# Optimization experiments

Measured on AMD Instinct MI355X. Metric: run time of the kernel, lower is better.

The kernel has to match this reference:

```python
import jax, jax.numpy as jnp
import numpy as np

B, T, H, E = 8, 2048, 512, 512

def setup_inputs() -> dict:
    key = jax.random.key(0)
    k1, k2, k3, k4 = jax.random.split(key, 4)
    tokens = jax.random.normal(k1, (B, T, H), dtype=jnp.float32)
    # Linear(hidden,embed,bias=False): stored as (in,out) so Q = tokens @ Wq
    Wq = jax.random.normal(k2, (H, E), dtype=jnp.float32) / np.sqrt(H)
    Wk = jax.random.normal(k3, (H, E), dtype=jnp.float32) / np.sqrt(H)
    Wv = jax.random.normal(k4, (H, H), dtype=jnp.float32) / np.sqrt(H)
    return {"tokens": tokens, "Wq": Wq, "Wk": Wk, "Wv": Wv}

def reference(tokens, Wq, Wk, Wv):
    Q = jnp.einsum('bth,he->bte', tokens, Wq)   # [B,T,E]
    K = jnp.einsum('bsh,he->bse', tokens, Wk)   # [B,T,E]
    V = jnp.einsum('bsh,hd->bsd', tokens, Wv)   # [B,T,H]
    scoremats = jnp.einsum('bte,bse->bts', Q, K)  # [B,T,T]
    # NOTE: softmax over axis=1 (query axis t), matching F.softmax(dim=1)
    attnmats = jax.nn.softmax(scoremats, axis=1)
    ctx_vecs = jnp.einsum('bts,bsh->bth', attnmats, V)  # [B,T,H]
    return ctx_vecs
```

## Files before the change

kernel.cpp:

```cpp
#include <hip/hip_runtime.h>

typedef _Float16 f16;
typedef _Float16 f16x8 __attribute__((ext_vector_type(8)));
typedef _Float16 f16x4 __attribute__((ext_vector_type(4)));
typedef float   f32x4 __attribute__((ext_vector_type(4)));

#define LOG2E 1.44269504088896340736f

__device__ __forceinline__ f32x4 mfma_f16(f16x8 a, f16x8 b, f32x4 c){
  return __builtin_amdgcn_mfma_f32_16x16x32_f16(a, b, c, 0, 0, 0);
}
__device__ __forceinline__ float fexp2(float x){ return __builtin_amdgcn_exp2f(x); }

__device__ __forceinline__ void gld16(void* lds, const void* g){
  __builtin_amdgcn_global_load_lds(
      (const __attribute__((address_space(1))) unsigned int*)g,
      (__attribute__((address_space(3))) unsigned int*)lds,
      16, 0, 0);
}


__global__ __launch_bounds__(256) void k_prep_g(const float* __restrict__ Wq,
                                                const float* __restrict__ Wk,
                                                f16* __restrict__ B16){
  __shared__ float ak[32][36];
  __shared__ float aq[32][36];
  const int n0 = blockIdx.y * 32, e0 = blockIdx.x * 32;
  const int u = threadIdx.x;
  const int ty = u >> 4, tx = u & 15;
  float acc[2][2] = {};
  for (int x0 = 0; x0 < 512; x0 += 32){
    __syncthreads();
    {
      int r = u >> 3, c4 = (u & 7) * 4;
      *(float4*)&ak[r][c4] = *(const float4*)&Wk[(n0 + r) * 512 + x0 + c4];
      *(float4*)&aq[r][c4] = *(const float4*)&Wq[(e0 + r) * 512 + x0 + c4];
    }
    __syncthreads();
#pragma unroll 8
    for (int x = 0; x < 32; ++x){
      float k0 = ak[ty * 2 + 0][x], k1 = ak[ty * 2 + 1][x];
      float q0 = aq[tx * 2 + 0][x], q1 = aq[tx * 2 + 1][x];
      acc[0][0] += k0 * q0; acc[0][1] += k0 * q1;
      acc[1][0] += k1 * q0; acc[1][1] += k1 * q1;
    }
  }
#pragma unroll
  for (int i = 0; i < 2; ++i)
#pragma unroll
    for (int j = 0; j < 2; ++j)
      B16[(size_t)(n0 + ty * 2 + i) * 512 + e0 + tx * 2 + j] = (f16)acc[i][j];
}

__global__ __launch_bounds__(256) void k_prep_wv(const float* __restrict__ Wv,
                                                 f16* __restrict__ B16){
  __shared__ float t[64][72];
  const int e0 = blockIdx.x * 64, h0 = blockIdx.y * 64;
  const int u = threadIdx.x;
#pragma unroll
  for (int k = 0; k < 4; ++k){
    int idx = u + k * 256; int r = idx >> 4, c4 = (idx & 15) * 4;
    *(float4*)&t[r][c4] = *(const float4*)&Wv[(e0 + r) * 512 + h0 + c4];
  }
  __syncthreads();
#pragma unroll
  for (int k = 0; k < 4; ++k){
    int idx = u + k * 256; int j = idx >> 4, i4 = (idx & 15) * 4;
#pragma unroll
    for (int c = 0; c < 4; ++c)
      B16[(size_t)(512 + h0 + j) * 512 + e0 + i4 + c] = (f16)t[i4 + c][j];
  }
}

__global__ __launch_bounds__(256) void k_cast(const float* __restrict__ tok,
                                              f16* __restrict__ T16){
  int i = blockIdx.x * 256 + threadIdx.x;
  const float4* p = (const float4*)tok + (size_t)i * 2;
  float4 a = p[0], b = p[1];
  f16x8 h;
  h[0] = (f16)a.x; h[1] = (f16)a.y; h[2] = (f16)a.z; h[3] = (f16)a.w;
  h[4] = (f16)b.x; h[5] = (f16)b.y; h[6] = (f16)b.z; h[7] = (f16)b.w;
  *((f16x8*)T16 + i) = h;
}

__global__ __launch_bounds__(256, 4) void k_gemm(const f16* __restrict__ T16,
                                                 const f16* __restrict__ B16,
                                                 f16* __restrict__ QG,
                                                 f16* __restrict__ VT){
  __shared__ __align__(16) f16 Abuf[2][128 * 32];
  __shared__ __align__(16) f16 Bbuf[2][128 * 32];
  const int tb = blockIdx.x, nb = blockIdx.y;
  const int u = threadIdx.x;
  const int w = u >> 6, l = u & 63, lr = l & 15, lq = l >> 4;
  const int sxor = (l & 3) ^ ((l >> 3) & 3), hi4 = l >> 2;
  const int wm = (w & 1) * 64, wn = (w >> 1) * 64;
  f32x4 acc[4][4] = {};
  auto stage = [&](int c, int buf){
    const f16* sa = T16 + (size_t)tb * 128 * 512 + c * 32;
    const f16* sb = B16 + (size_t)nb * 128 * 512 + c * 32;
#pragma unroll
    for (int k = 0; k < 2; ++k){
      int i = w * 2 + k;
      int row = i * 16 + hi4;
      gld16((char*)&Abuf[buf][0] + i * 1024, sa + (size_t)row * 512 + sxor * 8);
      gld16((char*)&Bbuf[buf][0] + i * 1024, sb + (size_t)row * 512 + sxor * 8);
    }
  };
  stage(0, 0);
  for (int c = 0; c < 16; ++c){
    __syncthreads();
    if (c < 15) stage(c + 1, (c + 1) & 1);
    const f16* A = &Abuf[c & 1][0];
    const f16* B = &Bbuf[c & 1][0];
    f16x8 af[4], bf[4];
#pragma unroll
    for (int mt = 0; mt < 4; ++mt){
      int row = wm + mt * 16 + lr;
      af[mt] = *(const f16x8*)((const char*)A + row * 64 + (((lq ^ ((row >> 1) & 3))) << 4));
    }
#pragma unroll
    for (int nt = 0; nt < 4; ++nt){
      int row = wn + nt * 16 + lr;
      bf[nt] = *(const f16x8*)((const char*)B + row * 64 + (((lq ^ ((row >> 1) & 3))) << 4));
    }
#pragma unroll
    for (int mt = 0; mt < 4; ++mt)
#pragma unroll
      for (int nt = 0; nt < 4; ++nt)
        acc[mt][nt] = mfma_f16(af[mt], bf[nt], acc[mt][nt]);
  }
  if (nb < 4){
#pragma unroll
    for (int mt = 0; mt < 4; ++mt)
#pragma unroll
      for (int nt = 0; nt < 4; ++nt){
        int n = nb * 128 + wn + nt * 16 + lr;
        int r0 = tb * 128 + wm + mt * 16 + lq * 4;
#pragma unroll
        for (int j = 0; j < 4; ++j)
          QG[(size_t)(r0 + j) * 512 + n] = (f16)acc[mt][nt][j];
      }
  } else {
#pragma unroll
    for (int mt = 0; mt < 4; ++mt)
#pragma unroll
      for (int nt = 0; nt < 4; ++nt){
        int h = (nb - 4) * 128 + wn + nt * 16 + lr;
        int r0 = tb * 128 + wm + mt * 16 + lq * 4;
        int bq = r0 >> 11, s = r0 & 2047;
        f16x4 hv;
#pragma unroll
        for (int j = 0; j < 4; ++j) hv[j] = (f16)acc[mt][nt][j];
        *(f16x4*)&VT[(size_t)(bq * 512 + h) * 2048 + s] = hv;
      }
  }
}

__global__ __launch_bounds__(256, 4) void k_pass1p(const f16* __restrict__ T16,
                                                   const f16* __restrict__ QG,
                                                   f16* __restrict__ Pp,
                                                   float* __restrict__ Mp,
                                                   float* __restrict__ Dp){
  const int gid = blockIdx.x;
  const int b = gid & 7;
  const int sb = (gid >> 3) & 15;
  const int tb = gid >> 7;
  const int u = threadIdx.x;
  const int w = u >> 6, l = u & 63, lr = l & 15, lq = l >> 4;
  const int sxor = (l & 3) ^ ((l >> 3) & 3), hi4 = l >> 2;
  const int wm = (w & 1) * 64, wn = (w >> 1) * 64;

  __shared__ __align__(16) f16 Abuf[2][128 * 32];
  __shared__ __align__(16) f16 Bbuf[2][128 * 32];
  __shared__ float redM[2][128];
  __shared__ float redD[2][128];

  f32x4 acc[4][4] = {};
  const f16* sa0 = T16 + ((size_t)(b * 2048 + sb * 128) * 512);
  const f16* sb0 = QG + ((size_t)(b * 2048 + tb * 128) * 512);
  auto stage = [&](int c, int buf){
    const f16* sa = sa0 + c * 32;
    const f16* sb_ = sb0 + c * 32;
#pragma unroll
    for (int k = 0; k < 2; ++k){
      int i = w * 2 + k;
      int row = i * 16 + hi4;
      gld16((char*)&Abuf[buf][0] + i * 1024, sa  + (size_t)row * 512 + sxor * 8);
      gld16((char*)&Bbuf[buf][0] + i * 1024, sb_ + (size_t)row * 512 + sxor * 8);
    }
  };
  stage(0, 0);
  for (int c = 0; c < 16; ++c){
    __syncthreads();
    if (c < 15) stage(c + 1, (c + 1) & 1);
    const f16* A = &Abuf[c & 1][0];
    const f16* B = &Bbuf[c & 1][0];
    f16x8 af[4], bf[4];
#pragma unroll
    for (int mt = 0; mt < 4; ++mt){
      int row = wm + mt * 16 + lr;
      af[mt] = *(const f16x8*)((const char*)A + row * 64 + (((lq ^ ((row >> 1) & 3))) << 4));
    }
#pragma unroll
    for (int nt = 0; nt < 4; ++nt){
      int row = wn + nt * 16 + lr;
      bf[nt] = *(const f16x8*)((const char*)B + row * 64 + (((lq ^ ((row >> 1) & 3))) << 4));
    }
#pragma unroll
    for (int mt = 0; mt < 4; ++mt)
#pragma unroll
      for (int nt = 0; nt < 4; ++nt)
        acc[mt][nt] = mfma_f16(af[mt], bf[nt], acc[mt][nt]);
  }
#pragma unroll
  for (int mt = 0; mt < 4; ++mt)
#pragma unroll
    for (int nt = 0; nt < 4; ++nt)
#pragma unroll
      for (int j = 0; j < 4; ++j)
        acc[mt][nt][j] *= LOG2E;
#pragma unroll
  for (int mt = 0; mt < 4; ++mt)
#pragma unroll
    for (int j = 0; j < 4; ++j){
      float m2 = fmaxf(fmaxf(acc[mt][0][j], acc[mt][1][j]),
                       fmaxf(acc[mt][2][j], acc[mt][3][j]));
#pragma unroll
      for (int off = 1; off <= 8; off <<= 1)
        m2 = fmaxf(m2, __shfl_xor(m2, off, 64));
      if (lr == 0) redM[w >> 1][wm + mt * 16 + lq * 4 + j] = m2;
    }
  __syncthreads();
  float M[4][4];
#pragma unroll
  for (int mt = 0; mt < 4; ++mt)
#pragma unroll
    for (int j = 0; j < 4; ++j){
      int idx = wm + mt * 16 + lq * 4 + j;
      M[mt][j] = fmaxf(redM[0][idx], redM[1][idx]);
    }
#pragma unroll
  for (int mt = 0; mt < 4; ++mt)
#pragma unroll
    for (int nt = 0; nt < 4; ++nt){
      int t = tb * 128 + wn + nt * 16 + lr;
      f16x4 h4;
#pragma unroll
      for (int j = 0; j < 4; ++j){
        float p = fexp2(acc[mt][nt][j] - M[mt][j]);
        acc[mt][nt][j] = p;
        h4[j] = (f16)p;
      }
      *(f16x4*)&Pp[(size_t)(b * 2048 + t) * 2048 + sb * 128 + wm + mt * 16 + lq * 4] = h4;
    }
#pragma unroll
  for (int mt = 0; mt < 4; ++mt)
#pragma unroll
    for (int j = 0; j < 4; ++j){
      float sd = acc[mt][0][j] + acc[mt][1][j] + acc[mt][2][j] + acc[mt][3][j];
#pragma unroll
      for (int off = 1; off <= 8; off <<= 1)
        sd += __shfl_xor(sd, off, 64);
      if (lr == 0) redD[w >> 1][wm + mt * 16 + lq * 4 + j] = sd;
    }
  __syncthreads();
  if (u < 128){
    int sg = b * 2048 + sb * 128 + u;
    Mp[tb * 16384 + sg] = fmaxf(redM[0][u], redM[1][u]);
    Dp[tb * 16384 + sg] = redD[0][u] + redD[1][u];
  }
}

__global__ __launch_bounds__(256) void k_scm(const float* __restrict__ Mp,
                                             const float* __restrict__ Dp,
                                             f16* __restrict__ SC16){
  int i = blockIdx.x * 256 + threadIdx.x;
  float mv[16];
  float m = -1e30f;
#pragma unroll
  for (int ti = 0; ti < 16; ++ti){
    mv[ti] = Mp[ti * 16384 + i];
    m = fmaxf(m, mv[ti]);
  }
  float d = 0.f;
#pragma unroll
  for (int ti = 0; ti < 16; ++ti)
    d += Dp[ti * 16384 + i] * fexp2(mv[ti] - m);
  float rd = 1.0f / d;
#pragma unroll
  for (int ti = 0; ti < 16; ++ti)
    SC16[ti * 16384 + i] = (f16)(fexp2(mv[ti] - m) * rd);
}

__global__ __launch_bounds__(256, 2) void k_pass2p(const f16* __restrict__ Pp,
                                                   const f16* __restrict__ VT,
                                                   const f16* __restrict__ SC16,
                                                   float* __restrict__ out){
  const int gid = blockIdx.x;
  const int b = gid & 7;
  const int tb = (gid >> 3) & 15;
  const int hb = gid >> 7;
  const int u = threadIdx.x;
  const int w = u >> 6, l = u & 63, lr = l & 15, lq = l >> 4;
  const int sx8 = (l & 7) ^ (l >> 3), hi8 = l >> 3;
  const int wm = (w & 1) * 64, wn = (w >> 1) * 64;

  __shared__ __align__(16) f16 Abuf[2][128 * 64];
  __shared__ __align__(16) f16 Bbuf[2][128 * 64];
  __shared__ __align__(16) f16 scl[2048];

  {
    f16x8 v = *(const f16x8*)&SC16[(size_t)tb * 16384 + b * 2048 + u * 8];
    *(f16x8*)&scl[u * 8] = v;
  }
  f32x4 acc[4][4] = {};
  auto stage = [&](int c, int buf){
    const f16* sa = VT + ((size_t)(b * 512 + hb * 128) * 2048 + c * 64);
    const f16* sb_ = Pp + ((size_t)(b * 2048 + tb * 128) * 2048 + c * 64);
#pragma unroll
    for (int k = 0; k < 4; ++k){
      int i = w * 4 + k;
      int row = i * 8 + hi8;
      gld16((char*)&Abuf[buf][0] + i * 1024, sa  + (size_t)row * 2048 + sx8 * 8);
      gld16((char*)&Bbuf[buf][0] + i * 1024, sb_ + (size_t)row * 2048 + sx8 * 8);
    }
  };
  stage(0, 0);
  for (int c = 0; c < 32; ++c){
    __syncthreads();
    if (c < 31) stage(c + 1, (c + 1) & 1);
    const f16* A = &Abuf[c & 1][0];
    const f16* B = &Bbuf[c & 1][0];
#pragma unroll
    for (int es = 0; es < 2; ++es){
      f16x8 sclv = *(const f16x8*)&scl[c * 64 + es * 32 + lq * 8];
      f16x8 af[4], bf[4];
#pragma unroll
      for (int mt = 0; mt < 4; ++mt){
        int row = wm + mt * 16 + lr;
        af[mt] = *(const f16x8*)((const char*)A + row * 128 + (((es * 4 + lq) ^ (row & 7)) << 4));
      }
#pragma unroll
      for (int nt = 0; nt < 4; ++nt){
        int row = wn + nt * 16 + lr;
        f16x8 p = *(const f16x8*)((const char*)B + row * 128 + (((es * 4 + lq) ^ (row & 7)) << 4));
        bf[nt] = p * sclv;
      }
#pragma unroll
      for (int mt = 0; mt < 4; ++mt)
#pragma unroll
        for (int nt = 0; nt < 4; ++nt)
          acc[mt][nt] = mfma_f16(af[mt], bf[nt], acc[mt][nt]);
    }
  }
#pragma unroll
  for (int mt = 0; mt < 4; ++mt)
#pragma unroll
    for (int nt = 0; nt < 4; ++nt){
      int t = tb * 128 + wn + nt * 16 + lr;
      int h = hb * 128 + wm + mt * 16 + lq * 4;
      float4 v;
      v.x = acc[mt][nt][0]; v.y = acc[mt][nt][1];
      v.z = acc[mt][nt][2]; v.w = acc[mt][nt][3];
      *(float4*)&out[(size_t)(b * 2048 + t) * 512 + h] = v;
    }
}

extern "C" void kernel_launch(void* const* d_in, const int* in_sizes, int n_in,
                              void* d_out, int out_size, void* d_ws, size_t ws_size,
                              hipStream_t stream){
  (void)in_sizes; (void)n_in; (void)out_size; (void)ws_size;
  const float* tokens = (const float*)d_in[0];
  const float* Wq = (const float*)d_in[1];
  const float* Wk = (const float*)d_in[2];
  const float* Wv = (const float*)d_in[3];
  char* ws = (char*)d_ws;
  f16*    T16 = (f16*)(ws);
  f16*    QG  = (f16*)(ws + (16u << 20));
  f16*    VT  = (f16*)(ws + (32u << 20));
  f16*    B16 = (f16*)(ws + (48u << 20));
  f16*    SC16= (f16*)(ws + (50u << 20));
  float*  Mp  = (float*)(ws + (51u << 20));
  float*  Dp  = (float*)(ws + (52u << 20));
  f16*    Pp  = (f16*)(ws + (54u << 20));
  float* out = (float*)d_out;

  k_prep_g <<<dim3(16, 16), dim3(256), 0, stream>>>(Wq, Wk, B16);
  k_prep_wv<<<dim3(8, 8),   dim3(256), 0, stream>>>(Wv, B16);
  k_cast   <<<dim3(4096),   dim3(256), 0, stream>>>(tokens, T16);
  k_gemm   <<<dim3(128, 8), dim3(256), 0, stream>>>(T16, B16, QG, VT);
  k_pass1p <<<dim3(2048),   dim3(256), 0, stream>>>(T16, QG, Pp, Mp, Dp);
  k_scm    <<<dim3(64),     dim3(256), 0, stream>>>(Mp, Dp, SC16);
  k_pass2p <<<dim3(512),    dim3(256), 0, stream>>>(Pp, VT, SC16, out);
}
```

Before: 168.2 us.

## Merge prep kernels into one launch and use single-buffered 64-wide K chunks in pass1

The three preprocessing kernels (token cast, Wk·Wq^T product, Wv transpose) are merged into one launch that dispatches on block index, removing two kernel launches and their gaps. In k_pass1p the double-buffered 32-wide K staging is replaced by a single buffer holding 64-wide chunks with an 8-way XOR swizzle. This halves the number of K iterations but adds a second barrier per chunk. Global loads now no longer overlap with MFMA work inside a block, so the change relies on occupancy across blocks to hide load latency.

Result: slower. 175.9 us (+4.6%).

```diff
diff --git a/kernel.cpp b/kernel.cpp
--- a/kernel.cpp
+++ b/kernel.cpp
@@ -20,67 +20,69 @@
 }
 
 
-__global__ __launch_bounds__(256) void k_prep_g(const float* __restrict__ Wq,
-                                                const float* __restrict__ Wk,
-                                                f16* __restrict__ B16){
-  __shared__ float ak[32][36];
-  __shared__ float aq[32][36];
-  const int n0 = blockIdx.y * 32, e0 = blockIdx.x * 32;
+__global__ __launch_bounds__(256) void k_prep(const float* __restrict__ tok,
+                                              const float* __restrict__ Wq,
+                                              const float* __restrict__ Wk,
+                                              const float* __restrict__ Wv,
+                                              f16* __restrict__ B16,
+                                              f16* __restrict__ T16){
+  __shared__ __align__(16) float smem[64 * 72];
+  const int gb = blockIdx.x;
   const int u = threadIdx.x;
-  const int ty = u >> 4, tx = u & 15;
-  float acc[2][2] = {};
-  for (int x0 = 0; x0 < 512; x0 += 32){
-    __syncthreads();
-    {
-      int r = u >> 3, c4 = (u & 7) * 4;
-      *(float4*)&ak[r][c4] = *(const float4*)&Wk[(n0 + r) * 512 + x0 + c4];
-      *(float4*)&aq[r][c4] = *(const float4*)&Wq[(e0 + r) * 512 + x0 + c4];
-    }
-    __syncthreads();
+  if (gb < 4096){
+    int i = gb * 256 + u;
+    const float4* p = (const float4*)tok + (size_t)i * 2;
+    float4 a = p[0], b = p[1];
+    f16x8 h;
+    h[0] = (f16)a.x; h[1] = (f16)a.y; h[2] = (f16)a.z; h[3] = (f16)a.w;
+    h[4] = (f16)b.x; h[5] = (f16)b.y; h[6] = (f16)b.z; h[7] = (f16)b.w;
+    *((f16x8*)T16 + i) = h;
+  } else if (gb < 4352){
+    const int g2 = gb - 4096;
+    const int n0 = (g2 >> 4) * 32, e0 = (g2 & 15) * 32;
+    float (*ak)[36] = (float(*)[36])smem;
+    float (*aq)[36] = (float(*)[36])(smem + 32 * 36);
+    const int ty = u >> 4, tx = u & 15;
+    float acc[2][2] = {};
+    for (int x0 = 0; x0 < 512; x0 += 32){
+      __syncthreads();
+      {
+        int r = u >> 3, c4 = (u & 7) * 4;
+        *(float4*)&ak[r][c4] = *(const float4*)&Wk[(n0 + r) * 512 + x0 + c4];
+        *(float4*)&aq[r][c4] = *(const float4*)&Wq[(e0 + r) * 512 + x0 + c4];
+      }
+      __syncthreads();
 #pragma unroll 8
-    for (int x = 0; x < 32; ++x){
-      float k0 = ak[ty * 2 + 0][x], k1 = ak[ty * 2 + 1][x];
-      float q0 = aq[tx * 2 + 0][x], q1 = aq[tx * 2 + 1][x];
-      acc[0][0] += k0 * q0; acc[0][1] += k0 * q1;
-      acc[1][0] += k1 * q0; acc[1][1] += k1 * q1;
-    }
-  }
-#pragma unroll
-  for (int i = 0; i < 2; ++i)
-#pragma unroll
-    for (int j = 0; j < 2; ++j)
-      B16[(size_t)(n0 + ty * 2 + i) * 512 + e0 + tx * 2 + j] = (f16)acc[i][j];
-}
-
-__global__ __launch_bounds__(256) void k_prep_wv(const float* __restrict__ Wv,
-                                                 f16* __restrict__ B16){
-  __shared__ float t[64][72];
-  const int e0 = blockIdx.x * 64, h0 = blockIdx.y * 64;
-  const int u = threadIdx.x;
-#pragma unroll
-  for (int k = 0; k < 4; ++k){
-    int idx = u + k * 256; int r = idx >> 4, c4 = (idx & 15) * 4;
-    *(float4*)&t[r][c4] = *(const float4*)&Wv[(e0 + r) * 512 + h0 + c4];
-  }
-  __syncthreads();
-#pragma unroll
-  for (int k = 0; k < 4; ++k){
-    int idx = u + k * 256; int j = idx >> 4, i4 = (idx & 15) * 4;
-#pragma unroll
-    for (int c = 0; c < 4; ++c)
-      B16[(size_t)(512 + h0 + j) * 512 + e0 + i4 + c] = (f16)t[i4 + c][j];
-  }
-}
-
-__global__ __launch_bounds__(256) void k_cast(const float* __restrict__ tok,
-                                              f16* __restrict__ T16){
-  int i = blockIdx.x * 256 + threadIdx.x;
-  const float4* p = (const float4*)tok + (size_t)i * 2;
-  float4 a = p[0], b = p[1];
-  f16x8 h;
-  h[0] = (f16)a.x; h[1] = (f16)a.y; h[2] = (f16)a.z; h[3] = (f16)a.w;
-  h[4] = (f16)b.x; h[5] = (f16)b.y; h[6] = (f16)b.z; h[7] = (f16)b.w;
-  *((f16x8*)T16 + i) = h;
+      for (int x = 0; x < 32; ++x){
+        float k0 = ak[ty * 2 + 0][x], k1 = ak[ty * 2 + 1][x];
+        float q0 = aq[tx * 2 + 0][x], q1 = aq[tx * 2 + 1][x];
+        acc[0][0] += k0 * q0; acc[0][1] += k0 * q1;
+        acc[1][0] += k1 * q0; acc[1][1] += k1 * q1;
+      }
+    }
+#pragma unroll
+    for (int i = 0; i < 2; ++i)
+#pragma unroll
+      for (int j = 0; j < 2; ++j)
+        B16[(size_t)(n0 + ty * 2 + i) * 512 + e0 + tx * 2 + j] = (f16)acc[i][j];
+  } else {
+    const int g3 = gb - 4352;
+    const int e0 = (g3 & 7) * 64, h0 = (g3 >> 3) * 64;
+    float (*t)[72] = (float(*)[72])smem;
+#pragma unroll
+    for (int k = 0; k < 4; ++k){
+      int idx = u + k * 256; int r = idx >> 4, c4 = (idx & 15) * 4;
+      *(float4*)&t[r][c4] = *(const float4*)&Wv[(e0 + r) * 512 + h0 + c4];
+    }
+    __syncthreads();
+#pragma unroll
+    for (int k = 0; k < 4; ++k){
+      int idx = u + k * 256; int j = idx >> 4, i4 = (idx & 15) * 4;
+#pragma unroll
+      for (int c = 0; c < 4; ++c)
+        B16[(size_t)(512 + h0 + j) * 512 + e0 + i4 + c] = (f16)t[i4 + c][j];
+    }
+  }
 }
 
 __global__ __launch_bounds__(256, 4) void k_gemm(const f16* __restrict__ T16,
@@ -167,50 +169,50 @@
   const int tb = gid >> 7;
   const int u = threadIdx.x;
   const int w = u >> 6, l = u & 63, lr = l & 15, lq = l >> 4;
-  const int sxor = (l & 3) ^ ((l >> 3) & 3), hi4 = l >> 2;
+  const int sx8 = (l & 7) ^ (l >> 3), hi8 = l >> 3;
   const int wm = (w & 1) * 64, wn = (w >> 1) * 64;
 
-  __shared__ __align__(16) f16 Abuf[2][128 * 32];
-  __shared__ __align__(16) f16 Bbuf[2][128 * 32];
+  __shared__ __align__(16) f16 Abuf[128 * 64];
+  __shared__ __align__(16) f16 Bbuf[128 * 64];
   __shared__ float redM[2][128];
   __shared__ float redD[2][128];
 
   f32x4 acc[4][4] = {};
   const f16* sa0 = T16 + ((size_t)(b * 2048 + sb * 128) * 512);
   const f16* sb0 = QG + ((size_t)(b * 2048 + tb * 128) * 512);
-  auto stage = [&](int c, int buf){
-    const f16* sa = sa0 + c * 32;
-    const f16* sb_ = sb0 + c * 32;
-#pragma unroll
-    for (int k = 0; k < 2; ++k){
-      int i = w * 2 + k;
-      int row = i * 16 + hi4;
-      gld16((char*)&Abuf[buf][0] + i * 1024, sa  + (size_t)row * 512 + sxor * 8);
-      gld16((char*)&Bbuf[buf][0] + i * 1024, sb_ + (size_t)row * 512 + sxor * 8);
-    }
-  };
-  stage(0, 0);
-  for (int c = 0; c < 16; ++c){
-    __syncthreads();
-    if (c < 15) stage(c + 1, (c + 1) & 1);
-    const f16* A = &Abuf[c & 1][0];
-    const f16* B = &Bbuf[c & 1][0];
-    f16x8 af[4], bf[4];
-#pragma unroll
-    for (int mt = 0; mt < 4; ++mt){
-      int row = wm + mt * 16 + lr;
-      af[mt] = *(const f16x8*)((const char*)A + row * 64 + (((lq ^ ((row >> 1) & 3))) << 4));
-    }
-#pragma unroll
-    for (int nt = 0; nt < 4; ++nt){
-      int row = wn + nt * 16 + lr;
-      bf[nt] = *(const f16x8*)((const char*)B + row * 64 + (((lq ^ ((row >> 1) & 3))) << 4));
-    }
-#pragma unroll
-    for (int mt = 0; mt < 4; ++mt)
-#pragma unroll
-      for (int nt = 0; nt < 4; ++nt)
-        acc[mt][nt] = mfma_f16(af[mt], bf[nt], acc[mt][nt]);
+  for (int c = 0; c < 8; ++c){
+    {
+      const f16* sa = sa0 + c * 64;
+      const f16* sb_ = sb0 + c * 64;
+#pragma unroll
+      for (int k = 0; k < 4; ++k){
+        int i = w * 4 + k;
+        int row = i * 8 + hi8;
+        gld16((char*)Abuf + i * 1024, sa  + (size_t)row * 512 + sx8 * 8);
+        gld16((char*)Bbuf + i * 1024, sb_ + (size_t)row * 512 + sx8 * 8);
+      }
+    }
+    __syncthreads();
+#pragma unroll
+    for (int es = 0; es < 2; ++es){
+      f16x8 af[4], bf[4];
+#pragma unroll
+      for (int mt = 0; mt < 4; ++mt){
+        int row = wm + mt * 16 + lr;
+        af[mt] = *(const f16x8*)((const char*)Abuf + row * 128 + (((es * 4 + lq) ^ (row & 7)) << 4));
+      }
+#pragma unroll
+      for (int nt = 0; nt < 4; ++nt){
+        int row = wn + nt * 16 + lr;
+        bf[nt] = *(const f16x8*)((const char*)Bbuf + row * 128 + (((es * 4 + lq) ^ (row & 7)) << 4));
+      }
+#pragma unroll
+      for (int mt = 0; mt < 4; ++mt)
+#pragma unroll
+        for (int nt = 0; nt < 4; ++nt)
+          acc[mt][nt] = mfma_f16(af[mt], bf[nt], acc[mt][nt]);
+    }
+    __syncthreads();
   }
 #pragma unroll
   for (int mt = 0; mt < 4; ++mt)
@@ -385,9 +387,7 @@
   f16*    Pp  = (f16*)(ws + (54u << 20));
   float* out = (float*)d_out;
 
-  k_prep_g <<<dim3(16, 16), dim3(256), 0, stream>>>(Wq, Wk, B16);
-  k_prep_wv<<<dim3(8, 8),   dim3(256), 0, stream>>>(Wv, B16);
-  k_cast   <<<dim3(4096),   dim3(256), 0, stream>>>(tokens, T16);
+  k_prep   <<<dim3(4416),   dim3(256), 0, stream>>>(tokens, Wq, Wk, Wv, B16, T16);
   k_gemm   <<<dim3(128, 8), dim3(256), 0, stream>>>(T16, B16, QG, VT);
   k_pass1p <<<dim3(2048),   dim3(256), 0, stream>>>(T16, QG, Pp, Mp, Dp);
   k_scm    <<<dim3(64),     dim3(256), 0, stream>>>(Mp, Dp, SC16);
```

## Widen pass1 tile to 128x256 with 512 threads and K-chunk 64

Applied to the files above, without the earlier changes.

The score/softmax-partial kernel now uses 512-thread blocks covering 256 query rows per block instead of 128. This halves the block count and the number of per-tile max/sum partials, and k_scm and k_pass2p are updated to read 8 partials. The K loop uses 64-wide chunks with a single LDS buffer and two barriers per chunk instead of double-buffered 32-wide chunks. The aim is more reuse of the token tile and fewer partials to combine, at the cost of losing copy/compute overlap inside a block.

Result: slower. 323.1 us (+92.1%).

```diff
diff --git a/kernel.cpp b/kernel.cpp
--- a/kernel.cpp
+++ b/kernel.cpp
@@ -156,7 +156,7 @@
   }
 }
 
-__global__ __launch_bounds__(256, 4) void k_pass1p(const f16* __restrict__ T16,
+__global__ __launch_bounds__(512, 6) void k_pass1p(const f16* __restrict__ T16,
                                                    const f16* __restrict__ QG,
                                                    f16* __restrict__ Pp,
                                                    float* __restrict__ Mp,
@@ -167,50 +167,56 @@
   const int tb = gid >> 7;
   const int u = threadIdx.x;
   const int w = u >> 6, l = u & 63, lr = l & 15, lq = l >> 4;
-  const int sxor = (l & 3) ^ ((l >> 3) & 3), hi4 = l >> 2;
-  const int wm = (w & 1) * 64, wn = (w >> 1) * 64;
-
-  __shared__ __align__(16) f16 Abuf[2][128 * 32];
-  __shared__ __align__(16) f16 Bbuf[2][128 * 32];
-  __shared__ float redM[2][128];
-  __shared__ float redD[2][128];
+  const int sx8 = (l & 7) ^ (l >> 3), hi8 = l >> 3;
+  const int ws2 = w & 1, wt2 = w >> 1;
+  const int wm = ws2 * 64, wn = wt2 * 64;
+
+  __shared__ __align__(16) f16 Abuf[128 * 64];
+  __shared__ __align__(16) f16 Bbuf[256 * 64];
+  __shared__ float redM[4][128];
+  __shared__ float redD[4][128];
 
   f32x4 acc[4][4] = {};
   const f16* sa0 = T16 + ((size_t)(b * 2048 + sb * 128) * 512);
-  const f16* sb0 = QG + ((size_t)(b * 2048 + tb * 128) * 512);
-  auto stage = [&](int c, int buf){
-    const f16* sa = sa0 + c * 32;
-    const f16* sb_ = sb0 + c * 32;
-#pragma unroll
-    for (int k = 0; k < 2; ++k){
-      int i = w * 2 + k;
-      int row = i * 16 + hi4;
-      gld16((char*)&Abuf[buf][0] + i * 1024, sa  + (size_t)row * 512 + sxor * 8);
-      gld16((char*)&Bbuf[buf][0] + i * 1024, sb_ + (size_t)row * 512 + sxor * 8);
-    }
-  };
-  stage(0, 0);
-  for (int c = 0; c < 16; ++c){
-    __syncthreads();
-    if (c < 15) stage(c + 1, (c + 1) & 1);
-    const f16* A = &Abuf[c & 1][0];
-    const f16* B = &Bbuf[c & 1][0];
-    f16x8 af[4], bf[4];
-#pragma unroll
-    for (int mt = 0; mt < 4; ++mt){
-      int row = wm + mt * 16 + lr;
-      af[mt] = *(const f16x8*)((const char*)A + row * 64 + (((lq ^ ((row >> 1) & 3))) << 4));
-    }
-#pragma unroll
-    for (int nt = 0; nt < 4; ++nt){
-      int row = wn + nt * 16 + lr;
-      bf[nt] = *(const f16x8*)((const char*)B + row * 64 + (((lq ^ ((row >> 1) & 3))) << 4));
-    }
-#pragma unroll
-    for (int mt = 0; mt < 4; ++mt)
-#pragma unroll
-      for (int nt = 0; nt < 4; ++nt)
-        acc[mt][nt] = mfma_f16(af[mt], bf[nt], acc[mt][nt]);
+  const f16* sb0 = QG + ((size_t)(b * 2048 + tb * 256) * 512);
+  for (int c = 0; c < 8; ++c){
+    {
+      const f16* sa = sa0 + c * 64;
+      const f16* sb_ = sb0 + c * 64;
+#pragma unroll
+      for (int k = 0; k < 2; ++k){
+        int i = w * 2 + k;
+        int row = i * 8 + hi8;
+        gld16((char*)Abuf + i * 1024, sa + (size_t)row * 512 + sx8 * 8);
+      }
+#pragma unroll
+      for (int k = 0; k < 4; ++k){
+        int i = w * 4 + k;
+        int row = i * 8 + hi8;
+        gld16((char*)Bbuf + i * 1024, sb_ + (size_t)row * 512 + sx8 * 8);
+      }
+    }
+    __syncthreads();
+#pragma unroll
+    for (int es = 0; es < 2; ++es){
+      f16x8 af[4], bf[4];
+#pragma unroll
+      for (int mt = 0; mt < 4; ++mt){
+        int row = wm + mt * 16 + lr;
+        af[mt] = *(const f16x8*)((const char*)Abuf + row * 128 + (((es * 4 + lq) ^ (row & 7)) << 4));
+      }
+#pragma unroll
+      for (int nt = 0; nt < 4; ++nt){
+        int row = wn + nt * 16 + lr;
+        bf[nt] = *(const f16x8*)((const char*)Bbuf + row * 128 + (((es * 4 + lq) ^ (row & 7)) << 4));
+      }
+#pragma unroll
+      for (int mt = 0; mt < 4; ++mt)
+#pragma unroll
+        for (int nt = 0; nt < 4; ++nt)
+          acc[mt][nt] = mfma_f16(af[mt], bf[nt], acc[mt][nt]);
+    }
+    __syncthreads();
   }
 #pragma unroll
   for (int mt = 0; mt < 4; ++mt)
@@ -228,7 +234,7 @@
 #pragma unroll
       for (int off = 1; off <= 8; off <<= 1)
         m2 = fmaxf(m2, __shfl_xor(m2, off, 64));
-      if (lr == 0) redM[w >> 1][wm + mt * 16 + lq * 4 + j] = m2;
+      if (lr == 0) redM[wt2][wm + mt * 16 + lq * 4 + j] = m2;
     }
   __syncthreads();
   float M[4][4];
@@ -237,13 +243,14 @@
 #pragma unroll
     for (int j = 0; j < 4; ++j){
       int idx = wm + mt * 16 + lq * 4 + j;
-      M[mt][j] = fmaxf(redM[0][idx], redM[1][idx]);
+      M[mt][j] = fmaxf(fmaxf(redM[0][idx], redM[1][idx]),
+                       fmaxf(redM[2][idx], redM[3][idx]));
     }
 #pragma unroll
   for (int mt = 0; mt < 4; ++mt)
 #pragma unroll
     for (int nt = 0; nt < 4; ++nt){
-      int t = tb * 128 + wn + nt * 16 + lr;
+      int t = tb * 256 + wn + nt * 16 + lr;
       f16x4 h4;
 #pragma unroll
       for (int j = 0; j < 4; ++j){
@@ -261,13 +268,14 @@
 #pragma unroll
       for (int off = 1; off <= 8; off <<= 1)
         sd += __shfl_xor(sd, off, 64);
-      if (lr == 0) redD[w >> 1][wm + mt * 16 + lq * 4 + j] = sd;
+      if (lr == 0) redD[wt2][wm + mt * 16 + lq * 4 + j] = sd;
     }
   __syncthreads();
   if (u < 128){
     int sg = b * 2048 + sb * 128 + u;
-    Mp[tb * 16384 + sg] = fmaxf(redM[0][u], redM[1][u]);
-    Dp[tb * 16384 + sg] = redD[0][u] + redD[1][u];
+    Mp[tb * 16384 + sg] = fmaxf(fmaxf(redM[0][u], redM[1][u]),
+                                fmaxf(redM[2][u], redM[3][u]));
+    Dp[tb * 16384 + sg] = redD[0][u] + redD[1][u] + redD[2][u] + redD[3][u];
   }
 }
 
@@ -275,20 +283,20 @@
                                              const float* __restrict__ Dp,
                                              f16* __restrict__ SC16){
   int i = blockIdx.x * 256 + threadIdx.x;
-  float mv[16];
+  float mv[8];
   float m = -1e30f;
 #pragma unroll
-  for (int ti = 0; ti < 16; ++ti){
+  for (int ti = 0; ti < 8; ++ti){
     mv[ti] = Mp[ti * 16384 + i];
     m = fmaxf(m, mv[ti]);
   }
   float d = 0.f;
 #pragma unroll
-  for (int ti = 0; ti < 16; ++ti)
+  for (int ti = 0; ti < 8; ++ti)
     d += Dp[ti * 16384 + i] * fexp2(mv[ti] - m);
   float rd = 1.0f / d;
 #pragma unroll
-  for (int ti = 0; ti < 16; ++ti)
+  for (int ti = 0; ti < 8; ++ti)
     SC16[ti * 16384 + i] = (f16)(fexp2(mv[ti] - m) * rd);
 }
 
@@ -300,6 +308,7 @@
   const int b = gid & 7;
   const int tb = (gid >> 3) & 15;
   const int hb = gid >> 7;
+  const int ti = tb >> 1;
   const int u = threadIdx.x;
   const int w = u >> 6, l = u & 63, lr = l & 15, lq = l >> 4;
   const int sx8 = (l & 7) ^ (l >> 3), hi8 = l >> 3;
@@ -310,7 +319,7 @@
   __shared__ __align__(16) f16 scl[2048];
 
   {
-    f16x8 v = *(const f16x8*)&SC16[(size_t)tb * 16384 + b * 2048 + u * 8];
+    f16x8 v = *(const f16x8*)&SC16[(size_t)ti * 16384 + b * 2048 + u * 8];
     *(f16x8*)&scl[u * 8] = v;
   }
   f32x4 acc[4][4] = {};
@@ -389,7 +398,7 @@
   k_prep_wv<<<dim3(8, 8),   dim3(256), 0, stream>>>(Wv, B16);
   k_cast   <<<dim3(4096),   dim3(256), 0, stream>>>(tokens, T16);
   k_gemm   <<<dim3(128, 8), dim3(256), 0, stream>>>(T16, B16, QG, VT);
-  k_pass1p <<<dim3(2048),   dim3(256), 0, stream>>>(T16, QG, Pp, Mp, Dp);
+  k_pass1p <<<dim3(1024),   dim3(512), 0, stream>>>(T16, QG, Pp, Mp, Dp);
   k_scm    <<<dim3(64),     dim3(256), 0, stream>>>(Mp, Dp, SC16);
   k_pass2p <<<dim3(512),    dim3(256), 0, stream>>>(Pp, VT, SC16, out);
 }
```
